# Performance work log

Hardware: AMD Instinct MI355X
Metric: run time of the kernel (lower is better)

## Reference

```python
import jax, jax.numpy as jnp
import numpy as np

B, S, E, P, H, F = 4, 4096, 256, 32, 8, 1024
DH = E // H
LN_EPS = 1e-5


def setup_inputs() -> dict:
    key = jax.random.key(0)
    ks = jax.random.split(key, 12)
    dt = jnp.float32
    return {
        "src": jax.random.normal(ks[0], (B, S, E), dt),
        "pos_embed": jax.random.normal(ks[1], (B, P, S), dt),
        # learnable positional transform (pos_linear: P -> P)
        "Wpos": jax.random.normal(ks[2], (P, P), dt) * (1.0 / np.sqrt(P)),
        "bpos": jnp.zeros((P,), dt),
        # RBF kernel hyperparameters (ScaleKernel(RBFKernel)) -- positive scalars
        "lengthscale": jnp.full((), 2.0, dt),
        "outputscale": jnp.full((), 1.0, dt),
        # value / output projections of multihead attention
        "Wv": jax.random.normal(ks[3], (E, E), dt) * (1.0 / np.sqrt(E)),
        "bv": jnp.zeros((E,), dt),
        "Wo": jax.random.normal(ks[4], (E, E), dt) * (1.0 / np.sqrt(E)),
        "bo": jnp.zeros((E,), dt),
        # feed-forward
        "W1": jax.random.normal(ks[5], (F, E), dt) * (1.0 / np.sqrt(E)),
        "b1": jnp.zeros((F,), dt),
        "W2": jax.random.normal(ks[6], (E, F), dt) * (1.0 / np.sqrt(F)),
        "b2": jnp.zeros((E,), dt),
        # layer norms
        "ln1_g": jnp.ones((E,), dt), "ln1_b": jnp.zeros((E,), dt),
        "ln2_g": jnp.ones((E,), dt), "ln2_b": jnp.zeros((E,), dt),
    }


def _layer_norm(x, g, b):
    mu = jnp.mean(x, -1, keepdims=True)
    var = jnp.mean(jnp.square(x - mu), -1, keepdims=True)
    return (x - mu) * jax.lax.rsqrt(var + LN_EPS) * g + b


def _rbf_scores(x, lengthscale, outputscale):
    # x: [B, S, P] -> scaled RBF kernel matrix [B, S, S]
    xs = x / lengthscale
    sq = jnp.sum(xs * xs, axis=-1)  # [B, S]
    d2 = sq[:, :, None] + sq[:, None, :] - 2.0 * jnp.einsum('bsp,btp->bst', xs, xs)
    d2 = jnp.maximum(d2, 0.0)
    return outputscale * jnp.exp(-0.5 * d2)


def reference(src, pos_embed, Wpos, bpos, lengthscale, outputscale,
              Wv, bv, Wo, bo, W1, b1, W2, b2, ln1_g, ln1_b, ln2_g, ln2_b):
    b, s, e = src.shape
    # learnable positional transform: [B,P,S] -> [B,S,P] -> linear -> back
    pe = jnp.einsum('bps,op->bos', pos_embed, Wpos) + bpos[None, :, None]  # [B,P,S]
    # GP-kernel attention scores over sequence positions
    scores = _rbf_scores(pe.transpose(0, 2, 1), lengthscale, outputscale)  # [B,S,S]
    attn = jax.nn.softmax(scores, axis=-1)
    # value projection, per-head weighted sum (scores shared across heads)
    v = (src @ Wv.T + bv).reshape(b, s, H, DH)
    ctx = jnp.einsum('bqk,bkhd->bqhd', attn, v).reshape(b, s, e)
    attn_out = ctx @ Wo.T + bo
    x = _layer_norm(src + attn_out, ln1_g, ln1_b)
    ff = jax.nn.relu(x @ W1.T + b1) @ W2.T + b2
    return _layer_norm(x + ff, ln2_g, ln2_b)
```

## Files before the change

kernel.cpp:

```cpp
#include <hip/hip_runtime.h>
#include <stdint.h>

#define BN 4
#define SN 4096
#define EN 256
#define PN 32
#define FN 1024
#define BS (BN*SN)
#define PAUG 64

typedef uint16_t bf16_t;
typedef short v4s  __attribute__((ext_vector_type(4)));
typedef short v8s  __attribute__((ext_vector_type(8)));
typedef __bf16 bf16x8 __attribute__((ext_vector_type(8)));
typedef float v4f   __attribute__((ext_vector_type(4)));
typedef float v16f  __attribute__((ext_vector_type(16)));

#define MFMA16(a,b,c) __builtin_amdgcn_mfma_f32_16x16x32_bf16(a,b,c,0,0,0)
#define MFMA32(a,b,c) __builtin_amdgcn_mfma_f32_32x32x16_bf16(a,b,c,0,0,0)

__device__ __forceinline__ float b2f(bf16_t x){
    uint32_t u = ((uint32_t)x) << 16; float f; __builtin_memcpy(&f, &u, 4); return f;
}
__device__ __forceinline__ bf16_t f2b(float f){
    uint32_t u; __builtin_memcpy(&u, &f, 4);
    u += 0x7FFFu + ((u >> 16) & 1u);
    return (bf16_t)(u >> 16);
}
__device__ __forceinline__ bf16x8 ldb8(const bf16_t* p){
    v8s r = *(const v8s*)p; return __builtin_bit_cast(bf16x8, r);
}
__device__ __forceinline__ bf16x8 ldb8u(const bf16_t* p){
    v4s lo = *(const v4s*)p;
    v4s hi = *(const v4s*)(p + 4);
    v8s r = __builtin_shufflevector(lo, hi, 0,1,2,3,4,5,6,7);
    return __builtin_bit_cast(bf16x8, r);
}
__device__ __forceinline__ float ldsc(const float* p){ return *p; }
__device__ __forceinline__ float ldsc(const bf16_t* p){ return b2f(*p); }
__device__ __forceinline__ void stsc(float* p, float v){ *p = v; }
__device__ __forceinline__ void stsc(bf16_t* p, float v){ *p = f2b(v); }

#if __has_builtin(__builtin_amdgcn_exp2f)
__device__ __forceinline__ float fexp2(float x){ return __builtin_amdgcn_exp2f(x); }
#else
__device__ __forceinline__ float fexp2(float x){ return exp2f(x); }
#endif

#if __has_builtin(__builtin_amdgcn_cvt_pk_bf16_f32)
typedef __bf16 bf16x2 __attribute__((ext_vector_type(2)));
__device__ __forceinline__ uint32_t pkbf16(float a, float b){
    bf16x2 r = __builtin_amdgcn_cvt_pk_bf16_f32(a, b);
    return __builtin_bit_cast(uint32_t, r);
}
#else
__device__ __forceinline__ uint32_t pkbf16(float a, float b){
    return (uint32_t)f2b(a) | ((uint32_t)f2b(b) << 16);
}
#endif

typedef const __attribute__((address_space(1))) uint32_t* glds_gp;
typedef __attribute__((address_space(3))) uint32_t* glds_lp;
__device__ __forceinline__ void glds16(const bf16_t* g, bf16_t* l){
    __builtin_amdgcn_global_load_lds((glds_gp)g, (glds_lp)l, 16, 0, 0);
}

__global__ __launch_bounds__(256) void prep_kernel(
    const float* __restrict__ src, bf16_t* __restrict__ srcb,
    const float* __restrict__ Wv, bf16_t* __restrict__ Wvb,
    const float* __restrict__ Wo, bf16_t* __restrict__ Wob,
    const float* __restrict__ W1, bf16_t* __restrict__ W1b,
    const float* __restrict__ W2, bf16_t* __restrict__ W2b,
    const float* __restrict__ pos, const float* __restrict__ Wp,
    const float* __restrict__ bp,  const float* __restrict__ lsp,
    bf16_t* __restrict__ xk, bf16_t* __restrict__ xq)
{
    __shared__ float Wsh[PN*PN];
    __shared__ float bsh[PN];
    int bid = blockIdx.x;
    int tid = threadIdx.x;

    if (bid < 4736){
        const float* sp; bf16_t* dp; int off;
        if (bid < 4096){ sp = src; dp = srcb; off = (bid*256 + tid)*4; }
        else {
            int i = ((bid - 4096)*256 + tid)*4;
            if      (i <  65536){ sp=Wv; dp=Wvb; off=i; }
            else if (i < 131072){ sp=Wo; dp=Wob; off=i- 65536; }
            else if (i < 393216){ sp=W1; dp=W1b; off=i-131072; }
            else                { sp=W2; dp=W2b; off=i-393216; }
        }
        float4 f = *(const float4*)(sp + off);
        v4s o;
        o.x = (short)f2b(f.x); o.y = (short)f2b(f.y);
        o.z = (short)f2b(f.z); o.w = (short)f2b(f.w);
        *(v4s*)(dp + off) = o;
        return;
    }

    int pb = bid - 4736;
    int b  = pb >> 4;
    int s  = (pb & 15)*256 + tid;

    for (int i = tid; i < PN*PN; i += 256) Wsh[i] = Wp[i];
    if (tid < PN) bsh[tid] = bp[tid];
    __syncthreads();

    float inv_ls = 1.0f / lsp[0];
    const float c1f = 1.4426950408889634f;

    float col[PN];
    #pragma unroll
    for (int p = 0; p < PN; p++) col[p] = pos[((size_t)b*PN + p)*SN + s];

    uint16_t xb[PN], qb[PN];
    float sq = 0.f;
    #pragma unroll 4
    for (int o = 0; o < PN; o++){
        float pe = bsh[o];
        #pragma unroll
        for (int p = 0; p < PN; p++) pe += col[p] * Wsh[o*PN + p];
        float pv = pe * inv_ls;
        uint16_t h = f2b(pv);
        xb[o] = h;
        qb[o] = f2b(c1f * pv);
        float xr = b2f(h);
        sq += xr * xr;
    }

    size_t base = ((size_t)b*SN + s) * PAUG;
    v8s pk[8];
    #pragma unroll
    for (int c = 0; c < 4; c++)
        #pragma unroll
        for (int j = 0; j < 8; j++) ((short*)&pk[c])[j] = (short)xb[c*8 + j];
    #pragma unroll
    for (int c = 4; c < 8; c++)
        #pragma unroll
        for (int j = 0; j < 8; j++) ((short*)&pk[c])[j] = 0;
    ((short*)&pk[4])[0] = (short)f2b(-0.5f * sq);
    ((short*)&pk[4])[1] = (short)0x3F80;
    #pragma unroll
    for (int c = 0; c < 8; c++) *(v8s*)(xk + base + c*8) = pk[c];

    #pragma unroll
    for (int c = 0; c < 4; c++)
        #pragma unroll
        for (int j = 0; j < 8; j++) ((short*)&pk[c])[j] = (short)qb[c*8 + j];
    ((short*)&pk[4])[0] = (short)f2b(c1f);
    ((short*)&pk[4])[1] = (short)f2b(-0.5f * sq * c1f);
    #pragma unroll
    for (int c = 0; c < 8; c++) *(v8s*)(xq + base + c*8) = pk[c];
}

template<int EPI, typename OutT>
__global__ __launch_bounds__(256) void gemm_t(
    const bf16_t* __restrict__ A, const bf16_t* __restrict__ W,
    const float* __restrict__ bias, OutT* __restrict__ out,
    bf16_t* __restrict__ vt, int N, int K)
{
    __shared__ __align__(16) bf16_t At[2][4096];
    __shared__ __align__(16) bf16_t Wt[2][4096];
    int tid = threadIdx.x;
    int lane = tid & 63, wv = tid >> 6, col = lane & 15, quad = lane >> 4;
    int m0 = blockIdx.x * 64, n0 = blockIdx.y * 64;
    int nck = K >> 6;

    int srow = tid >> 3;
    int spc  = (tid & 7) ^ (srow & 7);
    const bf16_t* asrc = A + (size_t)(m0 + srow)*K + spc*8;
    const bf16_t* wsrc = W + (size_t)(n0 + srow)*K + spc*8;

    v4f acc[4];
    #pragma unroll
    for (int t = 0; t < 4; t++) acc[t] = (v4f){0.f,0.f,0.f,0.f};

    glds16(asrc, &At[0][tid*8]);
    glds16(asrc + (size_t)32*K, &At[0][2048 + tid*8]);
    glds16(wsrc, &Wt[0][tid*8]);
    glds16(wsrc + (size_t)32*K, &Wt[0][2048 + tid*8]);
    __syncthreads();

    for (int c = 0; c < nck; c++){
        int cb = c & 1;
        if (c + 1 < nck){
            glds16(asrc + (c+1)*64, &At[cb^1][tid*8]);
            glds16(asrc + (size_t)32*K + (c+1)*64, &At[cb^1][2048 + tid*8]);
            glds16(wsrc + (c+1)*64, &Wt[cb^1][tid*8]);
            glds16(wsrc + (size_t)32*K + (c+1)*64, &Wt[cb^1][2048 + tid*8]);
        }
        #pragma unroll
        for (int kc = 0; kc < 2; kc++){
            int pc = ((kc*4 + quad) ^ (col & 7)) * 8;
            bf16x8 a = ldb8(&At[cb][(wv*16 + col)*64 + pc]);
            #pragma unroll
            for (int t = 0; t < 4; t++){
                bf16x8 b = ldb8(&Wt[cb][(t*16 + col)*64 + pc]);
                acc[t] = MFMA16(a, b, acc[t]);
            }
        }
        __syncthreads();
    }

    float bfv[4];
    #pragma unroll
    for (int t = 0; t < 4; t++) bfv[t] = bias[n0 + t*16 + col];

    if constexpr (EPI == 3){
        __shared__ uint16_t Tsh[64*74];
        #pragma unroll
        for (int r = 0; r < 4; r++)
            #pragma unroll
            for (int t = 0; t < 4; t++)
                Tsh[(wv*16 + quad*4 + r)*74 + t*16 + col] = f2b(acc[t][r] + bfv[t]);
        __syncthreads();
        int e = tid >> 2, sc = tid & 3;
        int b = m0 >> 12;
        int sbat = m0 & (SN-1);
        int eb   = (n0 + e) >> 5;
        int l31e = (n0 + e) & 31;
        int k16  = (sbat >> 4) + sc;
        v8s p0, p1;
        #pragma unroll
        for (int i = 0; i < 8; i++) ((short*)&p0)[i] = (short)Tsh[(sc*16 + i)*74 + e];
        #pragma unroll
        for (int i = 0; i < 8; i++) ((short*)&p1)[i] = (short)Tsh[(sc*16 + 8 + i)*74 + e];
        bf16_t* dst = vt + ((((size_t)b*8 + eb)*256 + k16)*64 + l31e)*8;
        *(v8s*)dst = p0;
        *(v8s*)(dst + 256) = p1;
    } else {
        #pragma unroll
        for (int r = 0; r < 4; r++){
            int row = m0 + wv*16 + quad*4 + r;
            #pragma unroll
            for (int t = 0; t < 4; t++){
                float y = acc[t][r] + bfv[t];
                if constexpr (EPI == 1) y = fmaxf(y, 0.f);
                stsc(out + (size_t)row*N + n0 + t*16 + col, y);
            }
        }
    }
}

template<typename OutT, typename ResT>
__global__ __launch_bounds__(256) void ln_kernel(
    const bf16_t* __restrict__ y, const ResT* __restrict__ res,
    const float* __restrict__ gamma, const float* __restrict__ beta,
    OutT* __restrict__ out)
{
    int tid = threadIdx.x;
    int row = blockIdx.x * 32 + (tid >> 3);
    int l8  = tid & 7;
    size_t base = (size_t)row * EN;
    float v[32];
    float s1 = 0.f, s2 = 0.f;
    #pragma unroll
    for (int i = 0; i < 4; i++){
        int off = l8*8 + i*64;
        v8s a = *(const v8s*)(y + base + off);
        #pragma unroll
        for (int j = 0; j < 8; j++){
            float t = b2f((bf16_t)(uint16_t)a[j]) + ldsc(res + base + off + j);
            v[i*8 + j] = t; s1 += t; s2 += t*t;
        }
    }
    #pragma unroll
    for (int m = 1; m <= 4; m <<= 1){
        s1 += __shfl_xor(s1, m);
        s2 += __shfl_xor(s2, m);
    }
    float mu = s1 * (1.f/256.f);
    float rs = rsqrtf(s2 * (1.f/256.f) - mu*mu + 1e-5f);
    #pragma unroll
    for (int i = 0; i < 4; i++){
        int off = l8*8 + i*64;
        #pragma unroll
        for (int j = 0; j < 8; j++)
            stsc(out + base + off + j, (v[i*8+j]-mu)*rs*gamma[off+j] + beta[off+j]);
    }
}

__global__ __launch_bounds__(512, 4) void attn_kernel(
    const bf16_t* __restrict__ xk, const bf16_t* __restrict__ xq,
    const bf16_t* __restrict__ vf, const float* __restrict__ osp,
    bf16_t* __restrict__ ctx)
{
    __shared__ __align__(16) bf16_t Wtb[2][32*132];
    __shared__ float densh[8][32];
    __shared__ float dent[32];

    int tid  = threadIdx.x;
    int lane = tid & 63;
    int wv   = tid >> 6;
    int col  = lane & 15;
    int quad = lane >> 4;
    int l31  = lane & 31;
    int half = lane >> 5;

    int bid = blockIdx.x;
    int b   = (bid & 7) >> 1;
    int qi  = ((bid >> 3) << 1) | (bid & 1);
    int q0  = qi * 32;

    float k2 = 1.4426950408889634f * osp[0];

    const bf16_t* xkb = xk + (size_t)b * SN * PAUG;
    const bf16_t* xqb = xq + (size_t)b * SN * PAUG;
    const bf16_t* vfb = vf + (((size_t)b*8 + wv)*256)*512 + lane*8;

    bf16x8 qf[2][2];
    #pragma unroll
    for (int g2 = 0; g2 < 2; g2++)
        #pragma unroll
        for (int h = 0; h < 2; h++)
            qf[g2][h] = ldb8(xqb + (size_t)(q0 + g2*16 + col)*PAUG + h*32 + quad*8);

    v16f acc;
    #pragma unroll
    for (int i = 0; i < 16; i++) acc[i] = 0.f;
    float den[2] = {0.f, 0.f};
    const v4f zero = (v4f){0.f,0.f,0.f,0.f};

    const bf16_t* krow0 = xkb + (size_t)(wv*16 + col)*PAUG + quad*8;
    bf16x8 kf0 = ldb8(krow0);
    bf16x8 kf1 = ldb8(krow0 + 32);

    for (int c = 0; c < 32; c++){
        int cb = c & 1;
        bf16x8 vr[8];
        #pragma unroll
        for (int subk = 0; subk < 8; subk++)
            vr[subk] = ldb8(vfb + (size_t)(c*8 + subk)*512);

        #pragma unroll
        for (int g2 = 0; g2 < 2; g2++){
            v4f st = MFMA16(kf0, qf[g2][0], zero);
            st = MFMA16(kf1, qf[g2][1], st);
            #pragma unroll
            for (int rp = 0; rp < 2; rp++){
                float w0 = fexp2(fmaf(k2, fexp2(st[rp*2+0]), -k2));
                float w1 = fexp2(fmaf(k2, fexp2(st[rp*2+1]), -k2));
                den[g2] += w0 + w1;
                *(uint32_t*)&Wtb[cb][(g2*16+col)*132 + wv*16 + quad*4 + rp*2] = pkbf16(w0, w1);
            }
        }
        __syncthreads();

        if (c + 1 < 32){
            const bf16_t* krow = xkb + (size_t)((c+1)*128 + wv*16 + col)*PAUG + quad*8;
            kf0 = ldb8(krow);
            kf1 = ldb8(krow + 32);
        }

        #pragma unroll
        for (int sk4 = 0; sk4 < 2; sk4++){
            bf16x8 af[4];
            #pragma unroll
            for (int j = 0; j < 4; j++)
                af[j] = ldb8u(&Wtb[cb][l31*132 + (sk4*4 + j)*16 + half*8]);
            #pragma unroll
            for (int j = 0; j < 4; j++)
                acc = MFMA32(af[j], vr[sk4*4 + j], acc);
        }
    }

    #pragma unroll
    for (int g2 = 0; g2 < 2; g2++){
        den[g2] += __shfl_xor(den[g2], 16);
        den[g2] += __shfl_xor(den[g2], 32);
    }
    if (lane < 16){
        densh[wv][lane]      = den[0];
        densh[wv][16 + lane] = den[1];
    }
    __syncthreads();
    if (tid < 32){
        float s = 0.f;
        #pragma unroll
        for (int w = 0; w < 8; w++) s += densh[w][tid];
        dent[tid] = 1.f / s;
    }
    __syncthreads();

    size_t obase = ((size_t)b*SN + q0) * EN + wv*32;
    #pragma unroll
    for (int rg = 0; rg < 16; rg++){
        int row = (rg & 3) + 8*(rg >> 2) + 4*half;
        float inv = dent[row];
        ctx[obase + (size_t)row*EN + l31] = f2b(acc[rg] * inv);
    }
}

extern "C" void kernel_launch(void* const* d_in, const int* in_sizes, int n_in,
                              void* d_out, int out_size, void* d_ws, size_t ws_size,
                              hipStream_t stream)
{
    (void)in_sizes; (void)n_in; (void)out_size; (void)ws_size;
    const float* src  = (const float*)d_in[0];
    const float* pos  = (const float*)d_in[1];
    const float* Wpos = (const float*)d_in[2];
    const float* bpos = (const float*)d_in[3];
    const float* ls   = (const float*)d_in[4];
    const float* os   = (const float*)d_in[5];
    const float* Wv   = (const float*)d_in[6];
    const float* bv   = (const float*)d_in[7];
    const float* Wo   = (const float*)d_in[8];
    const float* bo   = (const float*)d_in[9];
    const float* W1   = (const float*)d_in[10];
    const float* b1   = (const float*)d_in[11];
    const float* W2   = (const float*)d_in[12];
    const float* b2   = (const float*)d_in[13];
    const float* g1   = (const float*)d_in[14];
    const float* be1  = (const float*)d_in[15];
    const float* g2   = (const float*)d_in[16];
    const float* be2  = (const float*)d_in[17];

    char* w = (char*)d_ws;
    bf16_t* xkb  = (bf16_t*)(w);
    bf16_t* xqb  = (bf16_t*)(w + ( 2u<<20));
    bf16_t* Wvb  = (bf16_t*)(w + ( 4u<<20));
    bf16_t* Wob  = (bf16_t*)(w + ( 4u<<20) + (1u<<18));
    bf16_t* W1b  = (bf16_t*)(w + ( 5u<<20));
    bf16_t* W2b  = (bf16_t*)(w + ( 6u<<20));
    bf16_t* srcb = (bf16_t*)(w + ( 8u<<20));
    bf16_t* y2   = (bf16_t*)(w + ( 8u<<20));
    bf16_t* vtg  = (bf16_t*)(w + (16u<<20));
    bf16_t* y1   = (bf16_t*)(w + (16u<<20));
    bf16_t* ctx  = (bf16_t*)(w + (24u<<20));
    bf16_t* xws  = (bf16_t*)(w + (24u<<20));
    bf16_t* hws  = (bf16_t*)(w + (32u<<20));

    prep_kernel<<<dim3(4800), 256, 0, stream>>>(
        src, srcb, Wv, Wvb, Wo, Wob, W1, W1b, W2, W2b,
        pos, Wpos, bpos, ls, xkb, xqb);

    gemm_t<3, bf16_t><<<dim3(BS/64, EN/64), 256, 0, stream>>>(
        srcb, Wvb, bv, (bf16_t*)nullptr, vtg, EN, EN);
    attn_kernel<<<dim3(512), 512, 0, stream>>>(xkb, xqb, vtg, os, ctx);
    gemm_t<0, bf16_t><<<dim3(BS/64, EN/64), 256, 0, stream>>>(
        ctx, Wob, bo, y1, (bf16_t*)nullptr, EN, EN);
    ln_kernel<bf16_t, bf16_t><<<dim3(BS/32), 256, 0, stream>>>(y1, srcb, g1, be1, xws);
    gemm_t<1, bf16_t><<<dim3(BS/64, FN/64), 256, 0, stream>>>(
        xws, W1b, b1, hws, (bf16_t*)nullptr, FN, EN);
    gemm_t<0, bf16_t><<<dim3(BS/64, EN/64), 256, 0, stream>>>(
        hws, W2b, b2, y2, (bf16_t*)nullptr, EN, FN);
    ln_kernel<float, bf16_t><<<dim3(BS/32), 256, 0, stream>>>(y2, xws, g2, be2, (float*)d_out);
}
```

Measured before the change: 258.2 us.

## Double attention query tile to 64 rows to halve V reloads per key

```diff
diff --git a/kernel.cpp b/kernel.cpp
--- a/kernel.cpp
+++ b/kernel.cpp
@@ -280,14 +280,15 @@
     }
 }
 
-__global__ __launch_bounds__(512, 4) void attn_kernel(
+__global__ __launch_bounds__(512, 2) void attn_kernel(
     const bf16_t* __restrict__ xk, const bf16_t* __restrict__ xq,
     const bf16_t* __restrict__ vf, const float* __restrict__ osp,
     bf16_t* __restrict__ ctx)
 {
-    __shared__ __align__(16) bf16_t Wtb[2][32*132];
-    __shared__ float densh[8][32];
-    __shared__ float dent[32];
+    __shared__ __align__(16) bf16_t Wtb[2][64*260];
+    __shared__ __align__(16) bf16_t Qs[64*64];
+    __shared__ float densh[8][64];
+    __shared__ float dent[64];
 
     int tid  = threadIdx.x;
     int lane = tid & 63;
@@ -300,7 +301,7 @@
     int bid = blockIdx.x;
     int b   = (bid & 7) >> 1;
     int qi  = ((bid >> 3) << 1) | (bid & 1);
-    int q0  = qi * 32;
+    int q0  = qi * 64;
 
     float k2 = 1.4426950408889634f * osp[0];
 
@@ -308,73 +309,98 @@
     const bf16_t* xqb = xq + (size_t)b * SN * PAUG;
     const bf16_t* vfb = vf + (((size_t)b*8 + wv)*256)*512 + lane*8;
 
-    bf16x8 qf[2][2];
-    #pragma unroll
-    for (int g2 = 0; g2 < 2; g2++)
+    {
+        int qrow = tid >> 3;
+        int qpc  = (tid & 7) ^ (qrow & 7);
+        glds16(xqb + (size_t)(q0 + qrow)*PAUG + qpc*8, &Qs[tid*8]);
+    }
+
+    v16f acc[2];
+    #pragma unroll
+    for (int qg = 0; qg < 2; qg++)
+        #pragma unroll
+        for (int i = 0; i < 16; i++) acc[qg][i] = 0.f;
+    float den[4] = {0.f, 0.f, 0.f, 0.f};
+    const v4f zero = (v4f){0.f,0.f,0.f,0.f};
+
+    bf16x8 kf[2][2];
+    #pragma unroll
+    for (int kg = 0; kg < 2; kg++)
         #pragma unroll
         for (int h = 0; h < 2; h++)
-            qf[g2][h] = ldb8(xqb + (size_t)(q0 + g2*16 + col)*PAUG + h*32 + quad*8);
-
-    v16f acc;
-    #pragma unroll
-    for (int i = 0; i < 16; i++) acc[i] = 0.f;
-    float den[2] = {0.f, 0.f};
-    const v4f zero = (v4f){0.f,0.f,0.f,0.f};
-
-    const bf16_t* krow0 = xkb + (size_t)(wv*16 + col)*PAUG + quad*8;
-    bf16x8 kf0 = ldb8(krow0);
-    bf16x8 kf1 = ldb8(krow0 + 32);
-
-    for (int c = 0; c < 32; c++){
+            kf[kg][h] = ldb8(xkb + (size_t)(wv*32 + kg*16 + col)*PAUG + h*32 + quad*8);
+
+    __syncthreads();
+
+    for (int c = 0; c < 16; c++){
         int cb = c & 1;
-        bf16x8 vr[8];
-        #pragma unroll
-        for (int subk = 0; subk < 8; subk++)
-            vr[subk] = ldb8(vfb + (size_t)(c*8 + subk)*512);
-
-        #pragma unroll
-        for (int g2 = 0; g2 < 2; g2++){
-            v4f st = MFMA16(kf0, qf[g2][0], zero);
-            st = MFMA16(kf1, qf[g2][1], st);
-            #pragma unroll
-            for (int rp = 0; rp < 2; rp++){
-                float w0 = fexp2(fmaf(k2, fexp2(st[rp*2+0]), -k2));
-                float w1 = fexp2(fmaf(k2, fexp2(st[rp*2+1]), -k2));
-                den[g2] += w0 + w1;
-                *(uint32_t*)&Wtb[cb][(g2*16+col)*132 + wv*16 + quad*4 + rp*2] = pkbf16(w0, w1);
+        bf16x8 vr[16];
+        #pragma unroll
+        for (int sk = 0; sk < 16; sk++)
+            vr[sk] = ldb8(vfb + (size_t)(c*16 + sk)*512);
+
+        #pragma unroll
+        for (int qg = 0; qg < 2; qg++){
+            #pragma unroll
+            for (int g2 = 0; g2 < 2; g2++){
+                int qr = qg*32 + g2*16 + col;
+                bf16x8 qa = ldb8(&Qs[qr*64 + ((quad    ) ^ (col & 7))*8]);
+                bf16x8 qb = ldb8(&Qs[qr*64 + ((4 + quad) ^ (col & 7))*8]);
+                #pragma unroll
+                for (int kg = 0; kg < 2; kg++){
+                    v4f st = MFMA16(kf[kg][0], qa, zero);
+                    st = MFMA16(kf[kg][1], qb, st);
+                    #pragma unroll
+                    for (int rp = 0; rp < 2; rp++){
+                        float w0 = fexp2(fmaf(k2, fexp2(st[rp*2+0]), -k2));
+                        float w1 = fexp2(fmaf(k2, fexp2(st[rp*2+1]), -k2));
+                        den[qg*2+g2] += w0 + w1;
+                        *(uint32_t*)&Wtb[cb][qr*260 + wv*32 + kg*16 + quad*4 + rp*2]
+                            = pkbf16(w0, w1);
+                    }
+                }
             }
         }
         __syncthreads();
 
-        if (c + 1 < 32){
-            const bf16_t* krow = xkb + (size_t)((c+1)*128 + wv*16 + col)*PAUG + quad*8;
-            kf0 = ldb8(krow);
-            kf1 = ldb8(krow + 32);
-        }
-
-        #pragma unroll
-        for (int sk4 = 0; sk4 < 2; sk4++){
-            bf16x8 af[4];
-            #pragma unroll
-            for (int j = 0; j < 4; j++)
-                af[j] = ldb8u(&Wtb[cb][l31*132 + (sk4*4 + j)*16 + half*8]);
-            #pragma unroll
-            for (int j = 0; j < 4; j++)
-                acc = MFMA32(af[j], vr[sk4*4 + j], acc);
-        }
-    }
-
-    #pragma unroll
-    for (int g2 = 0; g2 < 2; g2++){
-        den[g2] += __shfl_xor(den[g2], 16);
-        den[g2] += __shfl_xor(den[g2], 32);
+        if (c + 1 < 16){
+            #pragma unroll
+            for (int kg = 0; kg < 2; kg++)
+                #pragma unroll
+                for (int h = 0; h < 2; h++)
+                    kf[kg][h] = ldb8(xkb + (size_t)((c+1)*256 + wv*32 + kg*16 + col)*PAUG
+                                     + h*32 + quad*8);
+        }
+
+        #pragma unroll
+        for (int qg = 0; qg < 2; qg++){
+            #pragma unroll
+            for (int sk4 = 0; sk4 < 4; sk4++){
+                bf16x8 af[4];
+                #pragma unroll
+                for (int j = 0; j < 4; j++)
+                    af[j] = ldb8u(&Wtb[cb][(qg*32 + l31)*260 + (sk4*4 + j)*16 + half*8]);
+                #pragma unroll
+                for (int j = 0; j < 4; j++)
+                    acc[qg] = MFMA32(af[j], vr[sk4*4 + j], acc[qg]);
+            }
+        }
+    }
+
+    #pragma unroll
+    for (int d = 0; d < 4; d++){
+        den[d] += __shfl_xor(den[d], 16);
+        den[d] += __shfl_xor(den[d], 32);
     }
     if (lane < 16){
-        densh[wv][lane]      = den[0];
-        densh[wv][16 + lane] = den[1];
+        #pragma unroll
+        for (int qg = 0; qg < 2; qg++)
+            #pragma unroll
+            for (int g2 = 0; g2 < 2; g2++)
+                densh[wv][qg*32 + g2*16 + lane] = den[qg*2+g2];
     }
     __syncthreads();
-    if (tid < 32){
+    if (tid < 64){
         float s = 0.f;
         #pragma unroll
         for (int w = 0; w < 8; w++) s += densh[w][tid];
@@ -384,10 +410,13 @@
 
     size_t obase = ((size_t)b*SN + q0) * EN + wv*32;
     #pragma unroll
-    for (int rg = 0; rg < 16; rg++){
-        int row = (rg & 3) + 8*(rg >> 2) + 4*half;
-        float inv = dent[row];
-        ctx[obase + (size_t)row*EN + l31] = f2b(acc[rg] * inv);
+    for (int qg = 0; qg < 2; qg++){
+        #pragma unroll
+        for (int rg = 0; rg < 16; rg++){
+            int row = (rg & 3) + 8*(rg >> 2) + 4*half;
+            float inv = dent[qg*32 + row];
+            ctx[obase + (size_t)(qg*32 + row)*EN + l31] = f2b(acc[qg][rg] * inv);
+        }
     }
 }
 
@@ -436,7 +465,7 @@
 
     gemm_t<3, bf16_t><<<dim3(BS/64, EN/64), 256, 0, stream>>>(
         srcb, Wvb, bv, (bf16_t*)nullptr, vtg, EN, EN);
-    attn_kernel<<<dim3(512), 512, 0, stream>>>(xkb, xqb, vtg, os, ctx);
+    attn_kernel<<<dim3(256), 512, 0, stream>>>(xkb, xqb, vtg, os, ctx);
     gemm_t<0, bf16_t><<<dim3(BS/64, EN/64), 256, 0, stream>>>(
         ctx, Wob, bo, y1, (bf16_t*)nullptr, EN, EN);
     ln_kernel<bf16_t, bf16_t><<<dim3(BS/32), 256, 0, stream>>>(y1, srcb, g1, be1, xws);
```

After: 243.0 us. 5.9% less time.
